# Kernel optimization log

Measured on AMD Instinct MI355X. Metric: run time of the kernel, lower is better.

## Reference

```python
import jax, jax.numpy as jnp
import numpy as np

KSIZE = 21
PAD = (KSIZE - 1) // 2
SCALE = 4
W0, W1, W2 = 1.0, 1.0, 1.0  # cfg.SOLVER.SR_LOSS_FUNC_SR_WEIGHT


def setup_inputs() -> dict:
    key = jax.random.key(0)
    ks = jax.random.split(key, 7)
    B, C, H, W = 16, 3, 512, 512
    return {
        "hr_pred": jax.random.normal(ks[0], (B, C, H, W), jnp.float32),
        "hr_target": jax.random.normal(ks[1], (B, C, H, W), jnp.float32),
        "lr_target": jax.random.normal(ks[2], (B, C, H // SCALE, W // SCALE), jnp.float32),
        "kernel_pred": jax.random.uniform(ks[3], (B, KSIZE * KSIZE, 64, 64), jnp.float32),
        "gt_kernel": jax.random.uniform(ks[4], (B, 1, KSIZE, KSIZE), jnp.float32),
        "segment_preds": jax.random.uniform(ks[5], (B, 1, H, W), jnp.float32),
        "segment_targets": jax.random.uniform(ks[6], (B, 1, H, W), jnp.float32),
        "iter": 1000,
    }


def _per_sample_blur(img, ker):
    # img: [C,H,W], ker: [k,k] -> depthwise conv with the same kernel on each channel
    C = img.shape[0]
    w = jnp.broadcast_to(ker[None, None], (C, 1, KSIZE, KSIZE))
    out = jax.lax.conv_general_dilated(
        img[None], w, window_strides=(1, 1),
        padding=[(PAD, PAD), (PAD, PAD)], feature_group_count=C)
    return out[0]


def _get_pseudo_lr(sr, kernel_feat):
    # GAP over spatial dims, normalize over channel dim -> per-sample blur kernel
    k = kernel_feat.mean(axis=(2, 3))                      # [B, k*k]
    k = k / k.sum(axis=1, keepdims=True)
    weight = k.reshape(k.shape[0], 1, KSIZE, KSIZE)        # [B,1,k,k]
    blurred = jax.vmap(_per_sample_blur)(sr, weight[:, 0])  # [B,C,H,W]
    B, C, H, W = blurred.shape
    lrs = jax.image.resize(blurred, (B, C, H // SCALE, W // SCALE), method="bicubic")
    return lrs, weight


def reference(hr_pred, hr_target, lr_target, kernel_pred, gt_kernel,
              segment_preds, segment_targets, iter):
    hr_loss = jnp.abs(hr_pred - hr_target)                 # L1, reduction='none'
    lr_pred, kernel_w = _get_pseudo_lr(hr_pred, kernel_pred)
    lr_loss = jnp.abs(lr_pred - lr_target)
    kernel_loss = jnp.square(kernel_w - gt_kernel)         # MSE, reduction='none'
    # ORIENTED_WEIGHT_ITER == -1 -> no crack/seg-fail weighting
    # ONLY_KERNEL_LOSS_FOR_PRETRAIN == False -> full weighted sum
    loss = (W0 * hr_loss.mean(axis=(1, 2, 3))
            + W1 * lr_loss.mean(axis=(1, 2, 3))
            + W2 * kernel_loss.mean(axis=(1, 2, 3)))       # [B]
    return loss, kernel_w
```

## Files before the change

kernel.cpp:

```cpp
#include <hip/hip_runtime.h>

#define NB 16
#define NC 3
#define NH 512
#define NW 512
#define TAPS 441
#define HL 128
#define WL 128

#define WS_KSUM   0
#define WS_WEIGHT 7056
#define WS_FCLASS 14112
#define WS_FPOLY  532512
#define WS_KLMEAN 560160
#define WS_HRPART 560176
#define WS_LRPOLY 561200
#define WS_LREDGE 561968
#define WS_TOTAL  574064
#define WS_LRB    574064
#define WS_W4     577000
#define WS_FPOLY2 3722728
#define WS_HRP2   3745256
#define WS_TOTAL4 3748328

__device__ inline float keysCubic(float x) {
  if (x < 1.f) return ((1.5f * x - 2.5f) * x) * x + 1.f;
  if (x < 2.f) return ((-0.5f * x + 2.5f) * x - 4.f) * x + 2.f;
  return 0.f;
}

__device__ inline float blockSumAll(float v, volatile float* red, int nw) {
  #pragma unroll
  for (int o = 32; o > 0; o >>= 1) v += __shfl_down(v, o, 64);
  int w = threadIdx.x >> 6, lane = threadIdx.x & 63;
  __syncthreads();
  if (lane == 0) red[w] = v;
  __syncthreads();
  float s = 0.f;
  for (int i = 0; i < nw; i++) s += red[i];
  return s;
}

__global__ void zero_accum(float* p, int n) {
  int t = blockIdx.x * blockDim.x + threadIdx.x;
  if (t < n) p[t] = 0.f;
}

__global__ void kmean_kernel(const float4* __restrict__ kp4, float* __restrict__ ksum) {
  __shared__ float red[4];
  int blk = blockIdx.x;
  int t = threadIdx.x;
  const float4* base = kp4 + (size_t)blk * 1024;
  float s = 0.f;
  #pragma unroll
  for (int i = 0; i < 4; i++) {
    float4 v = base[i * 256 + t];
    s += v.x + v.y + v.z + v.w;
  }
  float tot = blockSumAll(s, red, 4);
  if (t == 0) ksum[blk] = tot * (1.f / 4096.f);
}

__global__ void knorm_kernel(const float* __restrict__ ksum, const float* __restrict__ gt,
                             float* __restrict__ weight, float* __restrict__ kw_out,
                             float* __restrict__ kl_mean) {
  __shared__ float red[8];
  int b = blockIdx.x, t = threadIdx.x;
  float v = (t < TAPS) ? ksum[b * TAPS + t] : 0.f;
  float tot = blockSumAll(v, red, 8);
  float sq = 0.f;
  if (t < TAPS) {
    float w = v / tot;
    weight[b * TAPS + t] = w;
    kw_out[b * TAPS + t] = w;
    float d = w - gt[b * TAPS + t];
    sq = d * d;
  }
  float sqs = blockSumAll(sq, red, 8);
  if (t == 0) kl_mean[b] = sqs * (1.f / (float)TAPS);
}

__global__ void hrloss_kernel(const float4* __restrict__ a, const float4* __restrict__ bb,
                              float* __restrict__ hr_part) {
  __shared__ float red[4];
  int blk = blockIdx.x, t = threadIdx.x;
  int samp = blk >> 6, chunk = blk & 63;
  size_t base = (size_t)samp * 196608 + (size_t)chunk * 3072;
  float s = 0.f;
  #pragma unroll
  for (int i = 0; i < 12; i++) {
    float4 x = a[base + i * 256 + t];
    float4 y = bb[base + i * 256 + t];
    s += fabsf(x.x - y.x) + fabsf(x.y - y.y) + fabsf(x.z - y.z) + fabsf(x.w - y.w);
  }
  float tot = blockSumAll(s, red, 4);
  if (t == 0) hr_part[blk] = tot;
}

__global__ void precls_kernel(const float* __restrict__ ws_weight, float* __restrict__ fclass,
                              float* __restrict__ fpoly, float* __restrict__ fpoly2) {
  __shared__ float ker[441];
  __shared__ float H[21][36];
  __shared__ float Qy[16], Qx[16];
  int cy = blockIdx.x / 5, cx = blockIdx.x % 5, b = blockIdx.y;
  int t = threadIdx.x;
  for (int i = t; i < 441; i += 256) ker[i] = ws_weight[b * 441 + i];
  if (t == 0) {
    const int lo[5] = {6, 2, 0, 0, 0};
    const int hi[5] = {16, 16, 16, 14, 10};
    float s = 0.f;
    for (int k = 0; k < 16; k++) {
      float q = (k >= lo[cy] && k < hi[cy]) ? keysCubic(fabsf((float)k - 7.5f) * 0.25f) : 0.f;
      Qy[k] = q; s += q;
    }
    for (int k = 0; k < 16; k++) Qy[k] /= s;
    s = 0.f;
    for (int k = 0; k < 16; k++) {
      float q = (k >= lo[cx] && k < hi[cx]) ? keysCubic(fabsf((float)k - 7.5f) * 0.25f) : 0.f;
      Qx[k] = q; s += q;
    }
    for (int k = 0; k < 16; k++) Qx[k] /= s;
  }
  bool interior = (cy == 2 && cx == 2);
  if (interior) {
    for (int i = t; i < 1728; i += 256) fpoly[b * 1728 + i] = 0.f;
  }
  __syncthreads();
  for (int i = t; i < 756; i += 256) {
    int ty = i / 36, q = i - (i / 36) * 36;
    float s = 0.f;
    int tx0 = max(0, q - 15), tx1 = min(21, q + 1);
    for (int tx = tx0; tx < tx1; tx++) s += ker[ty * 21 + tx] * Qx[q - tx];
    H[ty][q] = s;
  }
  __syncthreads();
  float* Fb = fclass + ((size_t)b * 25 + (size_t)blockIdx.x) * 1296;
  for (int i = t; i < 1296; i += 256) {
    int p = i / 36, q = i - (i / 36) * 36;
    float s = 0.f;
    int ty0 = max(0, p - 15), ty1 = min(21, p + 1);
    for (int ty = ty0; ty < ty1; ty++) s += Qy[p - ty] * H[ty][q];
    Fb[i] = s;
    if (interior) {
      int phase = (p & 3) * 4 + (q & 3);
      fpoly[b * 1728 + phase * 108 + (p >> 2) * 12 + (q >> 2)] = s;
      if (fpoly2)
        fpoly2[b * 1408 + phase * 88 + (p >> 2) * 9 + (q >> 2)] = s;
    }
  }
}

__global__ __launch_bounds__(256, 5) void main_fused(const float* __restrict__ img,
                                                     const float* __restrict__ tgt,
                                                     const float* __restrict__ lr_tgt,
                                                     const float* __restrict__ fpoly2,
                                                     const float* __restrict__ fclass,
                                                     float* __restrict__ W4,
                                                     float* __restrict__ hrp,
                                                     float* __restrict__ lr_edge) {
  __shared__ __align__(16) float SM[7040];
  __shared__ float redh[4];
  int bid = blockIdx.x;
  int g = bid / 79, r = bid - g * 79;
  int t = threadIdx.x;

  if (r >= 16) {
    int eb = g * 63 + (r - 16);
    int bc = eb / 252, xblk = eb - bc * 252;
    int b = bc / 3;
    int wid = t >> 6, lane = t & 63;
    int idx = xblk * 4 + wid;
    int oy, ox;
    if (idx < 512) {
      int e = idx >> 7;
      oy = (e < 2) ? e : (124 + e);
      ox = idx & 127;
    } else {
      int j = idx - 512;
      oy = 2 + (j >> 2);
      int c = j & 3;
      ox = (c < 2) ? c : (124 + c);
    }
    int cy = (oy == 0) ? 0 : (oy == 1) ? 1 : (oy == 126) ? 3 : (oy == 127) ? 4 : 2;
    int cx = (ox == 0) ? 0 : (ox == 1) ? 1 : (ox == 126) ? 3 : (ox == 127) ? 4 : 2;
    const float* F = fclass + ((size_t)b * 25 + (size_t)(cy * 5 + cx)) * 1296;
    const float* imgbc = img + (size_t)bc * (NH * NW);
    int gy0 = 4 * oy - 16, gx0 = 4 * ox - 16;
    float acc = 0.f;
    #pragma unroll 3
    for (int tp = lane; tp < 1296; tp += 64) {
      int p = (unsigned)tp / 36u;
      int q = tp - p * 36;
      int gy = gy0 + p, gx = gx0 + q;
      float v = 0.f;
      if ((unsigned)gy < (unsigned)NH && (unsigned)gx < (unsigned)NW)
        v = imgbc[gy * NW + gx];
      acc = fmaf(F[tp], v, acc);
    }
    #pragma unroll
    for (int o = 32; o > 0; o >>= 1) acc += __shfl_down(acc, o, 64);
    __syncthreads();
    if (lane == 0) {
      float tv = lr_tgt[(size_t)bc * (HL * WL) + (size_t)oy * WL + ox];
      redh[wid] = fabsf(acc - tv);
    }
    __syncthreads();
    if (t == 0)
      lr_edge[bc * 252 + xblk] = redh[0] + redh[1] + redh[2] + redh[3];
    return;
  }

  int cb = g * 16 + r;
  int tileX = cb & 3, tileY = (cb >> 2) & 3, z = cb >> 4;
  int bc = z >> 2, phy = z & 3;
  int b = bc / 3;
  int phx = t >> 6;
  int pos = t & 63;
  int gy_ = pos >> 3;
  int gx_ = pos & 7;

  int rowBase = 128 * tileY - 16 + phy;
  int colBase = 128 * tileX - 16;
  const float* imgbc = img + (size_t)bc * (NH * NW);
  const float* tgtbc = tgt + (size_t)bc * (NH * NW);
  float l1 = 0.f;
  for (int idx = t; idx < 1600; idx += 256) {
    int yy = idx / 40, xx = idx - (idx / 40) * 40;
    int gy = rowBase + 4 * yy;
    int gx = colBase + 4 * xx;
    float4 v = {0.f, 0.f, 0.f, 0.f};
    if ((unsigned)gy < (unsigned)NH && (unsigned)gx < (unsigned)NW)
      v = *(const float4*)&imgbc[(size_t)gy * NW + gx];
    SM[0 * 1760 + yy * 44 + xx] = v.x;
    SM[1 * 1760 + yy * 44 + xx] = v.y;
    SM[2 * 1760 + yy * 44 + xx] = v.z;
    SM[3 * 1760 + yy * 44 + xx] = v.w;
    if (yy >= 4 && yy < 36 && xx >= 4 && xx < 36) {
      float4 tv = *(const float4*)&tgtbc[(size_t)gy * NW + gx];
      l1 += fabsf(v.x - tv.x) + fabsf(v.y - tv.y) + fabsf(v.z - tv.z) + fabsf(v.w - tv.w);
    }
  }
  __syncthreads();
  float hsum = blockSumAll(l1, redh, 4);
  if (t == 0) hrp[(z * 4 + tileY) * 4 + tileX] = hsum;

  float acc[4][4];
  #pragma unroll
  for (int rr = 0; rr < 4; rr++)
    #pragma unroll
    for (int j = 0; j < 4; j++) acc[rr][j] = 0.f;

  int foff = __builtin_amdgcn_readfirstlane(b * 1408 + (phy * 4 + phx) * 88);
  const float* fk = fpoly2 + foff;
  int smbase = __builtin_amdgcn_readfirstlane(phx * 1760);
  const float* Sp = &SM[smbase];
  #pragma unroll
  for (int m = 0; m < 12; m++) {
    const float* srow = &Sp[(4 * gy_ + m) * 44 + 4 * gx_];
    float4 a0 = *(const float4*)srow;
    float4 a1 = *(const float4*)(srow + 4);
    float4 a2 = *(const float4*)(srow + 8);
    float rowv[12] = {a0.x, a0.y, a0.z, a0.w, a1.x, a1.y, a1.z, a1.w,
                      a2.x, a2.y, a2.z, a2.w};
    #pragma unroll
    for (int rr = 0; rr < 4; rr++) {
      int uy = m - rr;
      if (uy >= 0 && uy < 9) {
        #pragma unroll
        for (int q = 0; q < 9; q++) {
          float fv = fk[uy * 9 + q];
          #pragma unroll
          for (int j = 0; j < 4; j++)
            acc[rr][j] = fmaf(fv, rowv[q + j], acc[rr][j]);
        }
      }
    }
  }

  __syncthreads();
  #pragma unroll
  for (int rr = 0; rr < 4; rr++) {
    float4 s = {acc[rr][0], acc[rr][1], acc[rr][2], acc[rr][3]};
    *(float4*)&SM[phx * 1024 + (4 * gy_ + rr) * 32 + 4 * gx_] = s;
  }
  __syncthreads();

  const float4* R0 = (const float4*)&SM[0];
  const float4* R1 = (const float4*)&SM[1024];
  const float4* R2 = (const float4*)&SM[2048];
  const float4* R3 = (const float4*)&SM[3072];
  float4 v0 = R0[t], v1 = R1[t], v2 = R2[t], v3 = R3[t];
  float4 s;
  s.x = v0.x + v1.x + v2.x + v3.x;
  s.y = v0.y + v1.y + v2.y + v3.y;
  s.z = v0.z + v1.z + v2.z + v3.z;
  s.w = v0.w + v1.w + v2.w + v3.w;

  int oy = 32 * tileY + (t >> 3);
  int ox = 32 * tileX + 4 * (t & 7);
  float* dst = W4 + ((size_t)phy * 48 + bc) * (HL * WL) + (size_t)oy * WL + ox;
  *(float4*)dst = s;
}

__global__ __launch_bounds__(256) void lrsum_kernel(const float* __restrict__ W4,
                                                    const float* __restrict__ lr_tgt,
                                                    float* __restrict__ lr_b) {
  __shared__ float red[4];
  int bc = blockIdx.y;
  int idx = blockIdx.x * 256 + threadIdx.x;
  float l = 0.f;
  if (idx < 15376) {
    int oy = 2 + idx / 124;
    int ox = 2 + (idx - (idx / 124) * 124);
    size_t base = (size_t)bc * (HL * WL) + (size_t)oy * WL + ox;
    const size_t PL = (size_t)48 * HL * WL;
    float s = W4[base] + W4[base + PL] + W4[base + 2 * PL] + W4[base + 3 * PL];
    l = fabsf(s - lr_tgt[base]);
  }
  float tot = blockSumAll(l, red, 4);
  if (threadIdx.x == 0) lr_b[bc * 61 + blockIdx.x] = tot;
}

__global__ __launch_bounds__(128) void fused_poly(const float* __restrict__ img,
                                                  const float* __restrict__ lr_tgt,
                                                  const float4* __restrict__ fpoly4,
                                                  float* __restrict__ lr_poly) {
  __shared__ __align__(16) float S[4][40][44];
  __shared__ float red[2];
  int tileX = blockIdx.x, tileY = blockIdx.y, bc = blockIdx.z;
  int b = bc / 3;
  int t = threadIdx.x;
  int oyT = t >> 2, oxG = t & 3;
  const float* imgbc = img + (size_t)bc * (NH * NW);
  const float4* fp4 = fpoly4 + b * 432;
  float acc[8] = {0.f, 0.f, 0.f, 0.f, 0.f, 0.f, 0.f, 0.f};
  int rowBase = 128 * tileY - 16;
  int colBase = 128 * tileX - 16;
  for (int phy = 0; phy < 4; phy++) {
    for (int idx = t; idx < 1600; idx += 128) {
      int yy = idx / 40, xx = idx - yy * 40;
      int gy = rowBase + 4 * yy + phy;
      int gx = colBase + 4 * xx;
      float4 v = {0.f, 0.f, 0.f, 0.f};
      if ((unsigned)gy < (unsigned)NH && (unsigned)gx < (unsigned)NW)
        v = *(const float4*)&imgbc[(size_t)gy * NW + gx];
      S[0][yy][xx] = v.x; S[1][yy][xx] = v.y; S[2][yy][xx] = v.z; S[3][yy][xx] = v.w;
    }
    __syncthreads();
    #pragma unroll
    for (int phx = 0; phx < 4; phx++) {
      const float4* fprow = fp4 + (phy * 4 + phx) * 27;
      for (int uy = 0; uy < 9; uy++) {
        const float* srow = &S[phx][oyT + uy][oxG * 8];
        float4 w0 = *(const float4*)(srow);
        float4 w1 = *(const float4*)(srow + 4);
        float4 w2 = *(const float4*)(srow + 8);
        float4 w3 = *(const float4*)(srow + 12);
        float w[16] = {w0.x, w0.y, w0.z, w0.w, w1.x, w1.y, w1.z, w1.w,
                       w2.x, w2.y, w2.z, w2.w, w3.x, w3.y, w3.z, w3.w};
        float4 f0 = fprow[uy * 3], f1 = fprow[uy * 3 + 1], f2 = fprow[uy * 3 + 2];
        float f[9] = {f0.x, f0.y, f0.z, f0.w, f1.x, f1.y, f1.z, f1.w, f2.x};
        #pragma unroll
        for (int q = 0; q < 9; q++) {
          #pragma unroll
          for (int r = 0; r < 8; r++) acc[r] = fmaf(f[q], w[q + r], acc[r]);
        }
      }
    }
    __syncthreads();
  }
  int oy = 32 * tileY + oyT;
  float l = 0.f;
  if (oy >= 2 && oy < 126) {
    const float* tg = lr_tgt + (size_t)bc * (HL * WL) + (size_t)oy * WL + 32 * tileX + oxG * 8;
    #pragma unroll
    for (int r = 0; r < 8; r++) {
      int ox = 32 * tileX + oxG * 8 + r;
      if (ox >= 2 && ox < 126) l += fabsf(acc[r] - tg[r]);
    }
  }
  float tot = blockSumAll(l, red, 2);
  if (t == 0) lr_poly[bc * 16 + tileY * 4 + tileX] = tot;
}

__global__ __launch_bounds__(256) void edge_kernel(const float* __restrict__ img,
                                                   const float* __restrict__ lr_tgt,
                                                   const float* __restrict__ fclass,
                                                   float* __restrict__ lr_edge) {
  __shared__ float red[4];
  int bc = blockIdx.y, b = bc / 3;
  int wid = threadIdx.x >> 6, lane = threadIdx.x & 63;
  int idx = blockIdx.x * 4 + wid;
  int oy, ox;
  if (idx < 512) {
    int e = idx >> 7;
    oy = (e < 2) ? e : (124 + e);
    ox = idx & 127;
  } else {
    int j = idx - 512;
    oy = 2 + (j >> 2);
    int c = j & 3;
    ox = (c < 2) ? c : (124 + c);
  }
  int cy = (oy == 0) ? 0 : (oy == 1) ? 1 : (oy == 126) ? 3 : (oy == 127) ? 4 : 2;
  int cx = (ox == 0) ? 0 : (ox == 1) ? 1 : (ox == 126) ? 3 : (ox == 127) ? 4 : 2;
  const float* F = fclass + ((size_t)b * 25 + (size_t)(cy * 5 + cx)) * 1296;
  const float* imgbc = img + (size_t)bc * (NH * NW);
  int gy0 = 4 * oy - 16, gx0 = 4 * ox - 16;
  float acc = 0.f;
  #pragma unroll 3
  for (int tp = lane; tp < 1296; tp += 64) {
    int p = (unsigned)tp / 36u;
    int q = tp - p * 36;
    int gy = gy0 + p, gx = gx0 + q;
    float v = 0.f;
    if ((unsigned)gy < (unsigned)NH && (unsigned)gx < (unsigned)NW)
      v = imgbc[gy * NW + gx];
    acc = fmaf(F[tp], v, acc);
  }
  #pragma unroll
  for (int o = 32; o > 0; o >>= 1) acc += __shfl_down(acc, o, 64);
  __syncthreads();
  if (lane == 0) {
    float tgt = lr_tgt[(size_t)bc * (HL * WL) + (size_t)oy * WL + ox];
    red[wid] = fabsf(acc - tgt);
  }
  __syncthreads();
  if (threadIdx.x == 0) {
    lr_edge[bc * 252 + blockIdx.x] = red[0] + red[1] + red[2] + red[3];
  }
}

__global__ void final_big4(const float* __restrict__ hrp, const float* __restrict__ lr_b,
                           const float* __restrict__ lr_edge, const float* __restrict__ kl_mean,
                           float* __restrict__ out) {
  __shared__ float red[4];
  int b = blockIdx.x, t = threadIdx.x;
  float hs = 0.f;
  for (int i = t; i < 192; i += 256) hs += hrp[b * 192 + i];
  float h = blockSumAll(hs, red, 4);
  float ls = 0.f;
  for (int i = t; i < 183; i += 256) ls += lr_b[b * 183 + i];
  for (int i = t; i < 756; i += 256) ls += lr_edge[b * 756 + i];
  float l = blockSumAll(ls, red, 4);
  if (t == 0)
    out[b] = h * (1.f / 786432.f) + l * (1.f / 49152.f) + kl_mean[b];
}

__global__ void final_reduce(const float* __restrict__ hr_part, const float* __restrict__ lr_poly,
                             const float* __restrict__ lr_edge, const float* __restrict__ kl_mean,
                             float* __restrict__ out) {
  __shared__ float red[4];
  int b = blockIdx.x, t = threadIdx.x;
  float hs = 0.f;
  for (int i = t; i < 64; i += 256) hs += hr_part[b * 64 + i];
  float h = blockSumAll(hs, red, 4);
  float ls = 0.f;
  for (int i = t; i < 48; i += 256) ls += lr_poly[b * 48 + i];
  for (int i = t; i < 756; i += 256) ls += lr_edge[b * 756 + i];
  float l = blockSumAll(ls, red, 4);
  if (t == 0)
    out[b] = h * (1.f / 786432.f) + l * (1.f / 49152.f) + kl_mean[b];
}

extern "C" void kernel_launch(void* const* d_in, const int* in_sizes, int n_in,
                              void* d_out, int out_size, void* d_ws, size_t ws_size,
                              hipStream_t stream) {
  const float* hr_pred = (const float*)d_in[0];
  const float* hr_target = (const float*)d_in[1];
  const float* lr_target = (const float*)d_in[2];
  const float* kernel_pred = (const float*)d_in[3];
  const float* gt_kernel = (const float*)d_in[4];
  float* out = (float*)d_out;
  float* ws = (float*)d_ws;

  bool big4 = ws_size >= (size_t)WS_TOTAL4 * sizeof(float);
  bool big = ws_size >= (size_t)WS_TOTAL * sizeof(float);
  float* ksum = ws + WS_KSUM;
  float* weight = ws + WS_WEIGHT;

  if (big) {
    float* fclass = ws + WS_FCLASS;
    float* fpoly = ws + WS_FPOLY;
    float* kl_mean = ws + WS_KLMEAN;
    float* lr_edge = ws + WS_LREDGE;
    float* fpoly2 = big4 ? (ws + WS_FPOLY2) : nullptr;
    kmean_kernel<<<NB * TAPS, 256, 0, stream>>>((const float4*)kernel_pred, ksum);
    knorm_kernel<<<NB, 512, 0, stream>>>(ksum, gt_kernel, weight, out + NB, kl_mean);
    precls_kernel<<<dim3(25, NB), 256, 0, stream>>>(weight, fclass, fpoly, fpoly2);
    if (big4) {
      float* lr_b = ws + WS_LRB;
      float* W4 = ws + WS_W4;
      float* hrp = ws + WS_HRP2;
      main_fused<<<79 * 192, 256, 0, stream>>>(hr_pred, hr_target, lr_target, fpoly2, fclass,
                                               W4, hrp, lr_edge);
      lrsum_kernel<<<dim3(61, NB * NC), 256, 0, stream>>>(W4, lr_target, lr_b);
      final_big4<<<NB, 256, 0, stream>>>(hrp, lr_b, lr_edge, kl_mean, out);
    } else {
      float* hr_part = ws + WS_HRPART;
      float* lr_poly = ws + WS_LRPOLY;
      hrloss_kernel<<<NB * 64, 256, 0, stream>>>((const float4*)hr_pred,
                                                 (const float4*)hr_target, hr_part);
      edge_kernel<<<dim3(252, NB * NC), 256, 0, stream>>>(hr_pred, lr_target, fclass, lr_edge);
      fused_poly<<<dim3(4, 4, NB * NC), 128, 0, stream>>>(hr_pred, lr_target,
                                                          (const float4*)fpoly, lr_poly);
      final_reduce<<<NB, 256, 0, stream>>>(hr_part, lr_poly, lr_edge, kl_mean, out);
    }
  } else {
    float* hr_sum = ws + 14112;
    float* lr_sum = hr_sum + 16;
    float* kl_mean = hr_sum + 32;
    zero_accum<<<1, 64, 0, stream>>>(hr_sum, 48);
    kmean_kernel<<<NB * TAPS, 256, 0, stream>>>((const float4*)kernel_pred, ksum);
    knorm_kernel<<<NB, 512, 0, stream>>>(ksum, gt_kernel, weight, out + NB, kl_mean);
    hrloss_kernel<<<NB * 64, 256, 0, stream>>>((const float4*)hr_pred, (const float4*)hr_target,
                                               ksum);
    final_reduce<<<NB, 256, 0, stream>>>(ksum, lr_sum, lr_sum, kl_mean, out);
  }
}
```

Baseline: 128.2 us.

## Move edge-pixel work from conv kernel into merged tail kernel with LR sum

The interior polyphase conv blocks and the border-pixel edge blocks were interleaved in one launch. They are now split: the conv kernel runs only interior tiles on a 3D grid, and the edge computation is merged with the LR-sum reduction into one tail kernel. The aim is to stop the heavy conv blocks and the gather-bound edge blocks from competing for the same wave slots, and to keep the same launch count by folding the reduction into the tail. The cost is that the edge work can no longer overlap with the conv phase and now runs serially after it.

After: 118.8 us. 1.08x faster.

```diff
diff --git a/kernel.cpp b/kernel.cpp
--- a/kernel.cpp
+++ b/kernel.cpp
@@ -150,70 +150,18 @@
   }
 }
 
-__global__ __launch_bounds__(256, 5) void main_fused(const float* __restrict__ img,
-                                                     const float* __restrict__ tgt,
-                                                     const float* __restrict__ lr_tgt,
-                                                     const float* __restrict__ fpoly2,
-                                                     const float* __restrict__ fclass,
-                                                     float* __restrict__ W4,
-                                                     float* __restrict__ hrp,
-                                                     float* __restrict__ lr_edge) {
+__global__ __launch_bounds__(256, 5) void conv_phase4f(const float* __restrict__ img,
+                                                       const float* __restrict__ tgt,
+                                                       const float* __restrict__ fpoly2,
+                                                       float* __restrict__ W4,
+                                                       float* __restrict__ hrp) {
   __shared__ __align__(16) float SM[7040];
   __shared__ float redh[4];
-  int bid = blockIdx.x;
-  int g = bid / 79, r = bid - g * 79;
-  int t = threadIdx.x;
-
-  if (r >= 16) {
-    int eb = g * 63 + (r - 16);
-    int bc = eb / 252, xblk = eb - bc * 252;
-    int b = bc / 3;
-    int wid = t >> 6, lane = t & 63;
-    int idx = xblk * 4 + wid;
-    int oy, ox;
-    if (idx < 512) {
-      int e = idx >> 7;
-      oy = (e < 2) ? e : (124 + e);
-      ox = idx & 127;
-    } else {
-      int j = idx - 512;
-      oy = 2 + (j >> 2);
-      int c = j & 3;
-      ox = (c < 2) ? c : (124 + c);
-    }
-    int cy = (oy == 0) ? 0 : (oy == 1) ? 1 : (oy == 126) ? 3 : (oy == 127) ? 4 : 2;
-    int cx = (ox == 0) ? 0 : (ox == 1) ? 1 : (ox == 126) ? 3 : (ox == 127) ? 4 : 2;
-    const float* F = fclass + ((size_t)b * 25 + (size_t)(cy * 5 + cx)) * 1296;
-    const float* imgbc = img + (size_t)bc * (NH * NW);
-    int gy0 = 4 * oy - 16, gx0 = 4 * ox - 16;
-    float acc = 0.f;
-    #pragma unroll 3
-    for (int tp = lane; tp < 1296; tp += 64) {
-      int p = (unsigned)tp / 36u;
-      int q = tp - p * 36;
-      int gy = gy0 + p, gx = gx0 + q;
-      float v = 0.f;
-      if ((unsigned)gy < (unsigned)NH && (unsigned)gx < (unsigned)NW)
-        v = imgbc[gy * NW + gx];
-      acc = fmaf(F[tp], v, acc);
-    }
-    #pragma unroll
-    for (int o = 32; o > 0; o >>= 1) acc += __shfl_down(acc, o, 64);
-    __syncthreads();
-    if (lane == 0) {
-      float tv = lr_tgt[(size_t)bc * (HL * WL) + (size_t)oy * WL + ox];
-      redh[wid] = fabsf(acc - tv);
-    }
-    __syncthreads();
-    if (t == 0)
-      lr_edge[bc * 252 + xblk] = redh[0] + redh[1] + redh[2] + redh[3];
-    return;
-  }
-
-  int cb = g * 16 + r;
-  int tileX = cb & 3, tileY = (cb >> 2) & 3, z = cb >> 4;
+  int z = blockIdx.z;
   int bc = z >> 2, phy = z & 3;
   int b = bc / 3;
+  int tileX = blockIdx.x, tileY = blockIdx.y;
+  int t = threadIdx.x;
   int phx = t >> 6;
   int pos = t & 63;
   int gy_ = pos >> 3;
@@ -242,13 +190,13 @@
   }
   __syncthreads();
   float hsum = blockSumAll(l1, redh, 4);
-  if (t == 0) hrp[(z * 4 + tileY) * 4 + tileX] = hsum;
+  if (t == 0) hrp[(blockIdx.z * 4 + blockIdx.y) * 4 + blockIdx.x] = hsum;
 
   float acc[4][4];
   #pragma unroll
-  for (int rr = 0; rr < 4; rr++)
+  for (int r = 0; r < 4; r++)
     #pragma unroll
-    for (int j = 0; j < 4; j++) acc[rr][j] = 0.f;
+    for (int j = 0; j < 4; j++) acc[r][j] = 0.f;
 
   int foff = __builtin_amdgcn_readfirstlane(b * 1408 + (phy * 4 + phx) * 88);
   const float* fk = fpoly2 + foff;
@@ -263,15 +211,15 @@
     float rowv[12] = {a0.x, a0.y, a0.z, a0.w, a1.x, a1.y, a1.z, a1.w,
                       a2.x, a2.y, a2.z, a2.w};
     #pragma unroll
-    for (int rr = 0; rr < 4; rr++) {
-      int uy = m - rr;
+    for (int r = 0; r < 4; r++) {
+      int uy = m - r;
       if (uy >= 0 && uy < 9) {
         #pragma unroll
         for (int q = 0; q < 9; q++) {
           float fv = fk[uy * 9 + q];
           #pragma unroll
           for (int j = 0; j < 4; j++)
-            acc[rr][j] = fmaf(fv, rowv[q + j], acc[rr][j]);
+            acc[r][j] = fmaf(fv, rowv[q + j], acc[r][j]);
         }
       }
     }
@@ -279,9 +227,9 @@
 
   __syncthreads();
   #pragma unroll
-  for (int rr = 0; rr < 4; rr++) {
-    float4 s = {acc[rr][0], acc[rr][1], acc[rr][2], acc[rr][3]};
-    *(float4*)&SM[phx * 1024 + (4 * gy_ + rr) * 32 + 4 * gx_] = s;
+  for (int r = 0; r < 4; r++) {
+    float4 s = {acc[r][0], acc[r][1], acc[r][2], acc[r][3]};
+    *(float4*)&SM[phx * 1024 + (4 * gy_ + r) * 32 + 4 * gx_] = s;
   }
   __syncthreads();
 
@@ -300,6 +248,75 @@
   int ox = 32 * tileX + 4 * (t & 7);
   float* dst = W4 + ((size_t)phy * 48 + bc) * (HL * WL) + (size_t)oy * WL + ox;
   *(float4*)dst = s;
+}
+
+__global__ __launch_bounds__(256) void tail_kernel(const float* __restrict__ img,
+                                                   const float* __restrict__ lr_tgt,
+                                                   const float* __restrict__ fclass,
+                                                   const float* __restrict__ W4,
+                                                   float* __restrict__ lr_edge,
+                                                   float* __restrict__ lr_b) {
+  __shared__ float red[4];
+  int bid = blockIdx.x;
+  int t = threadIdx.x;
+  if (bid < 12096) {
+    int bc = bid / 252, xblk = bid - bc * 252;
+    int b = bc / 3;
+    int wid = t >> 6, lane = t & 63;
+    int idx = xblk * 4 + wid;
+    int oy, ox;
+    if (idx < 512) {
+      int e = idx >> 7;
+      oy = (e < 2) ? e : (124 + e);
+      ox = idx & 127;
+    } else {
+      int j = idx - 512;
+      oy = 2 + (j >> 2);
+      int c = j & 3;
+      ox = (c < 2) ? c : (124 + c);
+    }
+    int cy = (oy == 0) ? 0 : (oy == 1) ? 1 : (oy == 126) ? 3 : (oy == 127) ? 4 : 2;
+    int cx = (ox == 0) ? 0 : (ox == 1) ? 1 : (ox == 126) ? 3 : (ox == 127) ? 4 : 2;
+    const float* F = fclass + ((size_t)b * 25 + (size_t)(cy * 5 + cx)) * 1296;
+    const float* imgbc = img + (size_t)bc * (NH * NW);
+    int gy0 = 4 * oy - 16, gx0 = 4 * ox - 16;
+    float acc = 0.f;
+    #pragma unroll 3
+    for (int tp = lane; tp < 1296; tp += 64) {
+      int p = (unsigned)tp / 36u;
+      int q = tp - p * 36;
+      int gy = gy0 + p, gx = gx0 + q;
+      float v = 0.f;
+      if ((unsigned)gy < (unsigned)NH && (unsigned)gx < (unsigned)NW)
+        v = imgbc[gy * NW + gx];
+      acc = fmaf(F[tp], v, acc);
+    }
+    #pragma unroll
+    for (int o = 32; o > 0; o >>= 1) acc += __shfl_down(acc, o, 64);
+    __syncthreads();
+    if (lane == 0) {
+      float tv = lr_tgt[(size_t)bc * (HL * WL) + (size_t)oy * WL + ox];
+      red[wid] = fabsf(acc - tv);
+    }
+    __syncthreads();
+    if (t == 0)
+      lr_edge[bc * 252 + xblk] = red[0] + red[1] + red[2] + red[3];
+  } else {
+    int j = bid - 12096;
+    int bc = j / 61, xblk = j - bc * 61;
+    int idx = xblk * 256 + t;
+    float l = 0.f;
+    if (idx < 15376) {
+      int oy = 2 + idx / 124;
+      int ox = 2 + (idx - (idx / 124) * 124);
+      size_t base = (size_t)bc * (HL * WL) + (size_t)oy * WL + ox;
+      const size_t PL = (size_t)48 * HL * WL;
+      float s = W4[base] + W4[base + PL] + W4[base + 2 * PL] + W4[base + 3 * PL];
+      l = fabsf(s - lr_tgt[base]);
+    }
+    float tot = blockSumAll(l, red, 4);
+    if (t == 0) lr_b[bc * 61 + xblk] = tot;
+  }
 }
 
 __global__ __launch_bounds__(256) void lrsum_kernel(const float* __restrict__ W4,
@@ -492,9 +509,10 @@
       float* lr_b = ws + WS_LRB;
       float* W4 = ws + WS_W4;
       float* hrp = ws + WS_HRP2;
-      main_fused<<<79 * 192, 256, 0, stream>>>(hr_pred, hr_target, lr_target, fpoly2, fclass,
-                                               W4, hrp, lr_edge);
-      lrsum_kernel<<<dim3(61, NB * NC), 256, 0, stream>>>(W4, lr_target, lr_b);
+      conv_phase4f<<<dim3(4, 4, NB * NC * 4), 256, 0, stream>>>(hr_pred, hr_target, fpoly2,
+                                                                W4, hrp);
+      tail_kernel<<<12096 + 2928, 256, 0, stream>>>(hr_pred, lr_target, fclass, W4,
+                                                    lr_edge, lr_b);
       final_big4<<<NB, 256, 0, stream>>>(hrp, lr_b, lr_edge, kl_mean, out);
     } else {
       float* hr_part = ws + WS_HRPART;
```
